# Performance work log

Measured on AMD Instinct MI355X. Metric: run time of the kernel, lower is better.

Reference implementation:

```python
import jax, jax.numpy as jnp
import numpy as np

PATCH_NUMS = (1, 2, 4, 8, 16)
BETA = 0.25
A = -0.75  # torch bicubic coefficient


def _cubic(s):
    s = abs(s)
    if s <= 1.0:
        return ((A + 2.0) * s - (A + 3.0)) * s * s + 1.0
    if s < 2.0:
        return (((s - 5.0) * s + 8.0) * s - 4.0) * A
    return 0.0


def bicubic_matrix(n_in, n_out):
    # Row-stochastic 1D resampling matrix matching torch upsample_bicubic2d
    # (align_corners=False: half-pixel centers, border index clamping).
    scale = n_in / n_out
    W = np.zeros((n_out, n_in), dtype=np.float32)
    for i in range(n_out):
        x = (i + 0.5) * scale - 0.5
        x0 = int(np.floor(x))
        t = x - x0
        for off in (-1, 0, 1, 2):
            idx = min(max(x0 + off, 0), n_in - 1)
            W[i, idx] += _cubic(t - off)
    return jnp.asarray(W)


def area_down(x, pn):
    # exact average pooling (h, w divisible by pn)
    b, c, h, w = x.shape
    kh, kw = h // pn, w // pn
    return x.reshape(b, c, pn, kh, pn, kw).mean(axis=(3, 5))


def bicubic_up(x, h_out, w_out):
    b, c, h_in, w_in = x.shape
    Wh = bicubic_matrix(h_in, h_out)  # (h_out, h_in)
    Ww = bicubic_matrix(w_in, w_out)  # (w_out, w_in)
    x = jnp.einsum('Oh,bchw->bcOw', Wh, x)
    x = jnp.einsum('Pw,bchw->bchP', Ww, x)
    return x


def vector_quantize(z, embed, beta):
    # z: (b,c,h,w); embed: (V,c)
    b, c, h, w = z.shape
    zf = z.transpose(0, 2, 3, 1).reshape(-1, c)  # (N,c)
    # squared L2 distances to codebook, (N,V)
    d = (zf * zf).sum(-1, keepdims=True) - 2.0 * zf @ embed.T + (embed * embed).sum(-1)
    idx = jnp.argmin(d, axis=1)  # (N,)
    zq = embed[idx].reshape(b, h, w, c).transpose(0, 3, 1, 2)
    sg = jax.lax.stop_gradient
    loss = beta * jnp.mean((sg(zq) - z) ** 2) + jnp.mean((zq - sg(z)) ** 2)
    zq_st = z + sg(zq - z)  # straight-through estimator
    return zq_st, idx.reshape(b, h, w), loss


def setup_inputs() -> dict:
    key = jax.random.key(0)
    k1, k2 = jax.random.split(key)
    z = jax.random.normal(k1, (256, 32, 16, 16), dtype=jnp.float32)
    embed = jax.random.normal(k2, (4096, 32), dtype=jnp.float32)
    return {"z": z, "embed": embed}


def reference(z, embed):
    b, c, h, w = z.shape
    f_rest = z
    f_hat = jnp.zeros_like(z)
    ms_idx = []
    vq_loss = jnp.float32(0.0)
    n = len(PATCH_NUMS)
    for i, pn in enumerate(PATCH_NUMS):
        z_scale = area_down(f_rest, pn) if i < n - 1 else f_rest
        z_q_scale, idx, loss_i = vector_quantize(z_scale, embed, BETA)
        z_q = bicubic_up(z_q_scale, h, w) if i < n - 1 else z_q_scale
        f_hat = f_hat + z_q
        f_rest = f_rest - z_q
        ms_idx.append(idx)
        vq_loss = vq_loss + loss_i
    vq_loss = vq_loss / n
    return (f_hat, *ms_idx, vq_loss)
```

## Files before the change

### kernel.cpp

```cpp
#include <hip/hip_runtime.h>
#include <hip/hip_bf16.h>
#include <cstdint>
#include <cstddef>


#define B_   256
#define V_   4096
#define NTOT 2097152
#define WIN  128
#define CAP  512
#define MARGIN_ 1.0f

using bf16x8 = __attribute__((ext_vector_type(8))) short;
using f32x4  = __attribute__((ext_vector_type(4))) float;

__device__ inline short f2bf(float f) {
  __hip_bfloat16 h = __float2bfloat16(f);
  return *reinterpret_cast<short*>(&h);
}
__device__ inline unsigned encf(float f) {
  unsigned u = __float_as_uint(f);
  return (u & 0x80000000u) ? ~u : (u | 0x80000000u);
}
__device__ inline float decf(unsigned u) {
  unsigned b = (u & 0x80000000u) ? (u ^ 0x80000000u) : ~u;
  return __uint_as_float(b);
}
__device__ inline int keyidx(unsigned long long k) {
  int i = (int)(unsigned)(k & 0xffffffffull);
  return min(max(i, 0), V_ - 1);
}
__device__ inline float min3f(float a, float b, float c) {
  float d;
  asm("v_min3_f32 %0, %1, %2, %3" : "=v"(d) : "v"(a), "v"(b), "v"(c));
  return d;
}

__global__ __launch_bounds__(256) void setup_kernel(
    const float* __restrict__ z, const float* __restrict__ embed,
    float* __restrict__ f_rest, float* __restrict__ zrow,
    short* __restrict__ zrowb, short* __restrict__ ebf,
    float* __restrict__ se, float* __restrict__ tables,
    float* __restrict__ loss_slots, unsigned long long* __restrict__ keys0,
    unsigned int* __restrict__ smin0)
{
  const int tid = threadIdx.x;
  const int t = blockIdx.x * 256 + tid;
  float v = z[t];
  f_rest[t] = v;

  __shared__ float sm[256];
  sm[tid] = v;
  __syncthreads();
  if (tid == 0) {
    float s = 0.f;
    for (int i = 0; i < 256; ++i) s += sm[i];
    int c = blockIdx.x & 31, b = blockIdx.x >> 5;
    float val = s * (1.0f / 256.0f);
    zrow[(size_t)b * 32 + c] = val;
    zrowb[(size_t)b * 32 + c] = f2bf(-val);
  }

  if (blockIdx.x < 16) {
    int code = blockIdx.x * 256 + tid;
    float s = 0.f;
#pragma unroll
    for (int c = 0; c < 32; ++c) {
      float e = embed[(size_t)code * 32 + c];
      ebf[(size_t)code * 32 + c] = f2bf(e);
      s += e * e;
    }
    se[code] = s;
  } else if (blockIdx.x == 16) {
    if (tid < 64) {
      int pn_i = tid >> 4;
      int o    = tid & 15;
      int pn   = 1 << pn_i;
      double scale = (double)pn / 16.0;
      double x  = (o + 0.5) * scale - 0.5;
      double x0 = floor(x);
      double tf = x - x0;
      float row[8];
#pragma unroll
      for (int h = 0; h < 8; ++h) row[h] = 0.f;
      const double A = -0.75;
#pragma unroll
      for (int off = -1; off <= 2; ++off) {
        double s = fabs(tf - (double)off);
        double cub;
        if (s <= 1.0)      cub = ((A + 2.0) * s - (A + 3.0)) * s * s + 1.0;
        else if (s < 2.0)  cub = (((s - 5.0) * s + 8.0) * s - 4.0) * A;
        else               cub = 0.0;
        int idx = (int)x0 + off;
        idx = min(max(idx, 0), pn - 1);
        row[idx] = (float)((double)row[idx] + cub);
      }
#pragma unroll
      for (int h = 0; h < 8; ++h) tables[pn_i * 128 + o * 8 + h] = row[h];
    }
  } else if (blockIdx.x == 17) {
    keys0[tid] = ~0ull;
    smin0[tid] = 0xFFFFFFFFu;
  } else if (blockIdx.x >= 20 && blockIdx.x < 60) {
    loss_slots[(blockIdx.x - 20) * 256 + tid] = 0.f;
  }
}

__global__ __launch_bounds__(256) void vq_phaseA_kernel(
    const short* __restrict__ zrowb, const short* __restrict__ ebf,
    const float* __restrict__ se, unsigned int* __restrict__ smin,
    int vchunk)
{
  __shared__ __align__(16) short elds[WIN * 40];
  __shared__ float selds[WIN];

  const int tid = threadIdx.x;
  const int lane = tid & 63, wave = tid >> 6;
  const int col = lane & 15, quad = lane >> 4;
  const int nw = blockIdx.x * 128 + wave * 32;
  const int vbase = blockIdx.y * vchunk;

  bf16x8 af[2];
#pragma unroll
  for (int f = 0; f < 2; ++f)
    af[f] = *(const bf16x8*)(zrowb + (size_t)(nw + f * 16 + col) * 32 + quad * 8);

  float mn[2][4];
#pragma unroll
  for (int f = 0; f < 2; ++f)
#pragma unroll
    for (int r = 0; r < 4; ++r) mn[f][r] = 3.4e38f;

  for (int w0 = 0; w0 < vchunk; w0 += WIN) {
    __syncthreads();
    {
      int row = tid >> 1, half = tid & 1;
      const bf16x8* src = (const bf16x8*)(ebf + (size_t)(vbase + w0 + row) * 32);
      bf16x8* dst = (bf16x8*)(elds + row * 40);
      dst[half * 2]     = src[half * 2];
      dst[half * 2 + 1] = src[half * 2 + 1];
      if (tid < WIN) selds[tid] = 0.5f * se[vbase + w0 + tid];
    }
    __syncthreads();
    for (int vv = 0; vv < WIN; vv += 16) {
      bf16x8 bf = *(const bf16x8*)(elds + (vv + col) * 40 + quad * 8);
      float sevh = selds[vv + col];
      f32x4 cin = {sevh, sevh, sevh, sevh};
#pragma unroll
      for (int f = 0; f < 2; ++f) {
        f32x4 d = __builtin_amdgcn_mfma_f32_16x16x32_bf16(af[f], bf, cin, 0, 0, 0);
#pragma unroll
        for (int r = 0; r < 4; ++r) mn[f][r] = fminf(mn[f][r], d[r]);
      }
    }
  }
#pragma unroll
  for (int f = 0; f < 2; ++f)
#pragma unroll
    for (int r = 0; r < 4; ++r) {
      float m = mn[f][r];
      m = fminf(m, __shfl_xor(m, 1, 64));
      m = fminf(m, __shfl_xor(m, 2, 64));
      m = fminf(m, __shfl_xor(m, 4, 64));
      m = fminf(m, __shfl_xor(m, 8, 64));
      mn[f][r] = m;
    }
  if (col == 0) {
#pragma unroll
    for (int f = 0; f < 2; ++f)
#pragma unroll
      for (int r = 0; r < 4; ++r)
        atomicMin(&smin[nw + f * 16 + quad * 4 + r], encf(mn[f][r]));
  }
}

__global__ __launch_bounds__(256) void vq_phaseB_kernel(
    const short* __restrict__ zrowb, const short* __restrict__ ebf,
    const float* __restrict__ se, const unsigned int* __restrict__ smin,
    const float* __restrict__ zrow, const float* __restrict__ embed,
    unsigned long long* __restrict__ keys, int vchunk, int nmax)
{
  __shared__ __align__(16) short elds[WIN * 40];
  __shared__ float selds[WIN];
  __shared__ unsigned long long clist[CAP];
  __shared__ int ccnt;

  const int tid = threadIdx.x;
  const int lane = tid & 63, wave = tid >> 6;
  const int col = lane & 15, quad = lane >> 4;
  const int nw = blockIdx.x * 128 + wave * 32;
  const int vbase = blockIdx.y * vchunk;

  if (tid == 0) ccnt = 0;
  __syncthreads();

  bf16x8 af[2];
#pragma unroll
  for (int f = 0; f < 2; ++f)
    af[f] = *(const bf16x8*)(zrowb + (size_t)(nw + f * 16 + col) * 32 + quad * 8);

  float thr[2][4];
#pragma unroll
  for (int f = 0; f < 2; ++f)
#pragma unroll
    for (int r = 0; r < 4; ++r)
      thr[f][r] = decf(smin[nw + f * 16 + quad * 4 + r]) + MARGIN_;
  float tmax = fmaxf(
      fmaxf(fmaxf(thr[0][0], thr[0][1]), fmaxf(thr[0][2], thr[0][3])),
      fmaxf(fmaxf(thr[1][0], thr[1][1]), fmaxf(thr[1][2], thr[1][3])));

  for (int w0 = 0; w0 < vchunk; w0 += WIN) {
    __syncthreads();
    {
      int row = tid >> 1, half = tid & 1;
      const bf16x8* src = (const bf16x8*)(ebf + (size_t)(vbase + w0 + row) * 32);
      bf16x8* dst = (bf16x8*)(elds + row * 40);
      dst[half * 2]     = src[half * 2];
      dst[half * 2 + 1] = src[half * 2 + 1];
      if (tid < WIN) selds[tid] = 0.5f * se[vbase + w0 + tid];
    }
    __syncthreads();
    for (int vv = 0; vv < WIN; vv += 16) {
      bf16x8 bf = *(const bf16x8*)(elds + (vv + col) * 40 + quad * 8);
      float sevh = selds[vv + col];
      f32x4 cin = {sevh, sevh, sevh, sevh};
      f32x4 dd[2];
      dd[0] = __builtin_amdgcn_mfma_f32_16x16x32_bf16(af[0], bf, cin, 0, 0, 0);
      dd[1] = __builtin_amdgcn_mfma_f32_16x16x32_bf16(af[1], bf, cin, 0, 0, 0);
      float a = min3f(dd[0][0], dd[0][1], dd[0][2]);
      float b = min3f(dd[0][3], dd[1][0], dd[1][1]);
      float c = min3f(dd[1][2], dd[1][3], a);
      if (fminf(b, c) <= tmax) {
#pragma unroll
        for (int f = 0; f < 2; ++f) {
#pragma unroll
          for (int r = 0; r < 4; ++r) {
            if (dd[f][r] <= thr[f][r]) {
              int n = nw + f * 16 + quad * 4 + r;
              int v = vbase + w0 + vv + col;
              int slot = atomicAdd(&ccnt, 1);
              if (slot < CAP) {
                clist[slot] =
                    ((unsigned long long)(unsigned)n << 32) | (unsigned)v;
              } else {
                const float* zp = zrow + (size_t)n * 32;
                const float* ep = embed + (size_t)v * 32;
                float dot = 0.f, sz = 0.f;
#pragma unroll 1
                for (int i = 0; i < 32; ++i) {
                  float zc = zp[i];
                  dot = fmaf(zc, ep[i], dot);
                  sz  = fmaf(zc, zc, sz);
                }
                float d = fmaf(-2.0f, dot, sz) + se[v];
                unsigned long long key =
                    ((unsigned long long)encf(d) << 32) | (unsigned)v;
                atomicMin(&keys[n], key);
              }
            }
          }
        }
      }
    }
  }

  __syncthreads();
  int tot = min(ccnt, CAP);
  for (int j = tid; j < tot; j += 256) {
    unsigned long long cv = clist[j];
    int n = min((int)(cv >> 32), nmax - 1);
    int v = min((int)(cv & 0xffffffffull), V_ - 1);
    const float* zp = zrow + (size_t)n * 32;
    const float* ep = embed + (size_t)v * 32;
    float dot = 0.f, sz = 0.f;
#pragma unroll
    for (int i = 0; i < 32; ++i) {
      float zc = zp[i];
      dot = fmaf(zc, ep[i], dot);
      sz  = fmaf(zc, zc, sz);
    }
    float d = fmaf(-2.0f, dot, sz) + se[v];
    unsigned long long key =
        ((unsigned long long)encf(d) << 32) | (unsigned)v;
    atomicMin(&keys[n], key);
  }
}

__global__ __launch_bounds__(256) void up_update_kernel(
    const float* __restrict__ embed, const unsigned long long* __restrict__ keys,
    const float* __restrict__ tbl, float* __restrict__ f_rest, int pn,
    float* __restrict__ zcol,
    unsigned long long* __restrict__ keys_nb, unsigned int* __restrict__ smin_nb,
    int pn_next, int n_next,
    float* __restrict__ idx_out, float* __restrict__ loss_slot)
{
  __shared__ float sm[256];
  __shared__ float sm_e[64];
  const int tid = threadIdx.x;
  const int t = blockIdx.x * 256 + tid;
  const int p = tid & 15, o = tid >> 4;
  const int c = blockIdx.x & 31, b = blockIdx.x >> 5;
  const int pn2 = pn * pn;

  float pre = f_rest[t];
  sm[tid] = pre;
  if (tid < pn2) {
    int idx = keyidx(keys[b * pn2 + tid]);
    if (c == 0) idx_out[b * pn2 + tid] = (float)idx;
    sm_e[tid] = embed[(size_t)idx * 32 + c];
  }
  __syncthreads();

  float lsum = 0.f;
  if (tid < pn2) {
    int k = 16 / pn;
    int ph = tid / pn, pw = tid - ph * pn;
    float s = 0.f;
    for (int i = 0; i < k; ++i)
      for (int j = 0; j < k; ++j)
        s += sm[(ph * k + i) * 16 + (pw * k + j)];
    float zavg = s * (1.0f / (k * k));
    float d = sm_e[tid] - zavg;
    lsum = d * d;
  }
#pragma unroll
  for (int off = 32; off > 0; off >>= 1) lsum += __shfl_down(lsum, off, 64);
  if ((tid & 63) == 0)
    atomicAdd(loss_slot + ((blockIdx.x & 127) << 4), lsum);

  const float* Wo = tbl + o * 8;
  const float* Wp = tbl + p * 8;
  float acc = 0.f;
  for (int w = 0; w < pn; ++w) {
    float inner = 0.f;
    for (int h = 0; h < pn; ++h)
      inner = fmaf(Wo[h], sm_e[h * pn + w], inner);
    acc = fmaf(Wp[w], inner, acc);
  }
  float nr = pre - acc;
  f_rest[t] = nr;

  __syncthreads();
  sm[tid] = nr;
  __syncthreads();
  const int pnn2 = pn_next * pn_next;
  if (tid < pnn2) {
    int ph = tid / pn_next, pw = tid - ph * pn_next;
    int k = 16 / pn_next;
    float s = 0.f;
    for (int i = 0; i < k; ++i)
      for (int j = 0; j < k; ++j)
        s += sm[(ph * k + i) * 16 + (pw * k + j)];
    float zavg = s * (1.0f / (k * k));
    zcol[(size_t)c * 65536 + b * pnn2 + tid] = zavg;
  }
  if (t < n_next) {
    keys_nb[t] = ~0ull;
    smin_nb[t] = 0xFFFFFFFFu;
  }
}

__global__ __launch_bounds__(256) void zpack_transpose_kernel(
    const float* __restrict__ zcol, float* __restrict__ zrow,
    short* __restrict__ zrowb)
{
  __shared__ float tile[64][33];
  const int tid = threadIdx.x;
  const int nb = blockIdx.x * 64;
  const int pt = tid & 63, cg = tid >> 6;
#pragma unroll
  for (int it = 0; it < 8; ++it) {
    int c = it * 4 + cg;
    tile[pt][c] = zcol[(size_t)c * 65536 + nb + pt];
  }
  __syncthreads();
  const int p = tid >> 2, q = tid & 3;
  float v[8];
#pragma unroll
  for (int k = 0; k < 8; ++k) v[k] = tile[p][q * 8 + k];
  float* op = zrow + (size_t)(nb + p) * 32 + q * 8;
  f32x4 lo = {v[0], v[1], v[2], v[3]};
  f32x4 hi = {v[4], v[5], v[6], v[7]};
  *(f32x4*)op = lo;
  *(f32x4*)(op + 4) = hi;
  bf16x8 bv;
#pragma unroll
  for (int k = 0; k < 8; ++k) bv[k] = f2bf(-v[k]);
  *(bf16x8*)(zrowb + (size_t)(nb + p) * 32 + q * 8) = bv;
}

__global__ __launch_bounds__(256) void final_add_kernel(
    const float* __restrict__ z, const float* __restrict__ f_rest,
    const float* __restrict__ embed, const unsigned long long* __restrict__ keys,
    float* __restrict__ f_hat, float* __restrict__ idx_out,
    float* __restrict__ loss_slot)
{
  const int tid = threadIdx.x;
  const int t = blockIdx.x * 256 + tid;
  const int c = blockIdx.x & 31, b = blockIdx.x >> 5;
  const int n = b * 256 + tid;
  int idx = keyidx(keys[n]);
  if (c == 0) idx_out[n] = (float)idx;
  float e = embed[(size_t)idx * 32 + c];
  float fr = f_rest[t];
  f_hat[t] = (z[t] - fr) + e;
  float d = e - fr;
  float lsum = d * d;
#pragma unroll
  for (int off = 32; off > 0; off >>= 1) lsum += __shfl_down(lsum, off, 64);
  if ((tid & 63) == 0)
    atomicAdd(loss_slot + ((blockIdx.x & 127) << 4), lsum);
}

__global__ __launch_bounds__(128) void loss_final_kernel(
    const float* __restrict__ loss_slots, float* __restrict__ out_loss)
{
  __shared__ float lred[2];
  const int tid = threadIdx.x;
  const float numel[5] = {8192.f, 32768.f, 131072.f, 524288.f, 2097152.f};
  float tot = 0.f;
  for (int s = 0; s < 5; ++s) {
    float x = loss_slots[s * 2048 + tid * 16];
#pragma unroll
    for (int off = 32; off > 0; off >>= 1) x += __shfl_down(x, off, 64);
    if ((tid & 63) == 0) lred[tid >> 6] = x;
    __syncthreads();
    if (tid == 0) {
      float m = (lred[0] + lred[1]) / numel[s];
      tot += 0.25f * m + m;
    }
    __syncthreads();
  }
  if (tid == 0) out_loss[0] = tot / 5.f;
}

extern "C" void kernel_launch(void* const* d_in, const int* in_sizes, int n_in,
                              void* d_out, int out_size, void* d_ws, size_t ws_size,
                              hipStream_t stream)
{
  const float* z     = (const float*)d_in[0];
  const float* embed = (const float*)d_in[1];
  float* out = (float*)d_out;
  float* ws  = (float*)d_ws;

  float* f_rest  = ws;
  float* zrow    = ws + 2097152;
  short* zrowb   = (short*)(ws + 4194304);
  short* ebf     = (short*)(ws + 5242880);
  float* se      = ws + 5308416;
  unsigned int* smin0 = (unsigned int*)(ws + 5312512);
  unsigned int* smin1 = (unsigned int*)(ws + 5378048);
  unsigned long long* keys0 = (unsigned long long*)(ws + 5394432);
  unsigned long long* keys1 = (unsigned long long*)(ws + 5525504);
  float* loss_slots = ws + 5558272;
  float* tables     = ws + 5568512;

  float* zcol = out;

  unsigned long long* keysb[2] = {keys0, keys1};
  unsigned int*       sminb[2] = {smin0, smin1};

  setup_kernel<<<NTOT / 256, 256, 0, stream>>>(z, embed, f_rest, zrow, zrowb,
                                               ebf, se, tables, loss_slots,
                                               keys0, smin0);

  const int PN[5]  = {1, 2, 4, 8, 16};
  const int NVC[5] = {32, 32, 32, 16, 16};
  int idx_off = NTOT;
  for (int i = 0; i < 5; ++i) {
    int pn = PN[i];
    int N  = B_ * pn * pn;
    int vchunk = V_ / NVC[i];
    unsigned long long* kb = keysb[i & 1];
    unsigned int*       sb = sminb[i & 1];
    dim3 g(N / 128, NVC[i]);
    vq_phaseA_kernel<<<g, 256, 0, stream>>>(zrowb, ebf, se, sb, vchunk);
    vq_phaseB_kernel<<<g, 256, 0, stream>>>(zrowb, ebf, se, sb, zrow, embed,
                                            kb, vchunk, N);
    if (i < 4) {
      int pnn = PN[i + 1];
      int n_next = B_ * pnn * pnn;
      up_update_kernel<<<NTOT / 256, 256, 0, stream>>>(
          embed, kb, tables + i * 128, f_rest, pn,
          zcol, keysb[(i + 1) & 1], sminb[(i + 1) & 1],
          pnn, n_next, out + idx_off, loss_slots + i * 2048);
      zpack_transpose_kernel<<<n_next / 64, 256, 0, stream>>>(zcol, zrow,
                                                              zrowb);
    } else {
      final_add_kernel<<<NTOT / 256, 256, 0, stream>>>(
          z, f_rest, embed, kb, out, out + idx_off, loss_slots + 4 * 2048);
    }
    idx_off += N;
  }
  loss_final_kernel<<<1, 128, 0, stream>>>(loss_slots, out + 2184448);
}
```

Before: 385.9 us.

## Compact candidate rows per vocab chunk before phase B on large scales

Phase A now also records each row's per-chunk minimum distance for the two largest scales. A new compaction kernel builds, per vocabulary chunk, a worklist of rows whose chunk minimum lies within the margin of the global minimum. A worklist-driven phase B then recomputes the MFMA distances only for those (row, chunk) pairs. This is meant to avoid redundant phase-B work on chunks that cannot hold the argmin, at the cost of an extra kernel launch, extra global writes, and atomics.

```diff
diff --git a/kernel.cpp b/kernel.cpp
--- a/kernel.cpp
+++ b/kernel.cpp
@@ -9,6 +9,7 @@
 #define NTOT 2097152
 #define WIN  128
 #define CAP  512
+#define CAPW 1024
 #define MARGIN_ 1.0f
 
 using bf16x8 = __attribute__((ext_vector_type(8))) short;
@@ -42,7 +43,7 @@
     short* __restrict__ zrowb, short* __restrict__ ebf,
     float* __restrict__ se, float* __restrict__ tables,
     float* __restrict__ loss_slots, unsigned long long* __restrict__ keys0,
-    unsigned int* __restrict__ smin0)
+    unsigned int* __restrict__ smin0, int* __restrict__ cnt0)
 {
   const int tid = threadIdx.x;
   const int t = blockIdx.x * 256 + tid;
@@ -101,6 +102,8 @@
   } else if (blockIdx.x == 17) {
     keys0[tid] = ~0ull;
     smin0[tid] = 0xFFFFFFFFu;
+  } else if (blockIdx.x == 18) {
+    if (tid < 32) cnt0[tid] = 0;
   } else if (blockIdx.x >= 20 && blockIdx.x < 60) {
     loss_slots[(blockIdx.x - 20) * 256 + tid] = 0.f;
   }
@@ -109,7 +112,7 @@
 __global__ __launch_bounds__(256) void vq_phaseA_kernel(
     const short* __restrict__ zrowb, const short* __restrict__ ebf,
     const float* __restrict__ se, unsigned int* __restrict__ smin,
-    int vchunk)
+    int vchunk, unsigned int* __restrict__ chunkmin, int N)
 {
   __shared__ __align__(16) short elds[WIN * 40];
   __shared__ float selds[WIN];
@@ -169,8 +172,12 @@
 #pragma unroll
     for (int f = 0; f < 2; ++f)
 #pragma unroll
-      for (int r = 0; r < 4; ++r)
-        atomicMin(&smin[nw + f * 16 + quad * 4 + r], encf(mn[f][r]));
+      for (int r = 0; r < 4; ++r) {
+        unsigned e = encf(mn[f][r]);
+        int n = nw + f * 16 + quad * 4 + r;
+        atomicMin(&smin[n], e);
+        if (chunkmin) chunkmin[(size_t)blockIdx.y * N + n] = e;
+      }
   }
 }
 
@@ -286,6 +293,147 @@
   }
 }
 
+__global__ __launch_bounds__(256) void compact_kernel(
+    const unsigned int* __restrict__ smin,
+    const unsigned int* __restrict__ chunkmin, int N, int nvc,
+    int* __restrict__ cnt, int* __restrict__ list)
+{
+  const int n = blockIdx.x * 256 + threadIdx.x;
+  const int lane = threadIdx.x & 63;
+  const float thr = decf(smin[n]) + MARGIN_;
+  for (int y = 0; y < nvc; ++y) {
+    bool q = decf(chunkmin[(size_t)y * N + n]) <= thr;
+    unsigned long long m = __ballot(q);
+    int base = 0;
+    if (lane == 0 && m) base = atomicAdd(&cnt[y], (int)__popcll(m));
+    base = __shfl(base, 0, 64);
+    if (q) {
+      int pos = base + (int)__popcll(m & ((1ull << lane) - 1ull));
+      list[(size_t)y * N + pos] = n;
+    }
+  }
+}
+
+__global__ __launch_bounds__(256) void vq_phaseB_wl_kernel(
+    const short* __restrict__ zrowb, const short* __restrict__ ebf,
+    const float* __restrict__ se, const unsigned int* __restrict__ smin,
+    const float* __restrict__ zrow, const float* __restrict__ embed,
+    unsigned long long* __restrict__ keys, int vchunk, int N,
+    const int* __restrict__ cnt, const int* __restrict__ list)
+{
+  __shared__ __align__(16) short elds[WIN * 40];
+  __shared__ float selds[WIN];
+  __shared__ unsigned long long clist[CAPW];
+  __shared__ int ptls[128];
+  __shared__ int ccnt;
+
+  const int tid = threadIdx.x;
+  const int lane = tid & 63, wave = tid >> 6;
+  const int col = lane & 15, quad = lane >> 4;
+  const int y = blockIdx.y;
+  const int vbase = y * vchunk;
+  const int total = cnt[y];
+
+  if (tid == 0) ccnt = 0;
+
+  for (int base = blockIdx.x * 128; base < total; base += gridDim.x * 128) {
+    __syncthreads();
+    if (tid < 128)
+      ptls[tid] = list[(size_t)y * N + min(base + tid, total - 1)];
+    __syncthreads();
+
+    bf16x8 af[2];
+    float thr[2][4];
+#pragma unroll
+    for (int f = 0; f < 2; ++f) {
+      int pm = ptls[wave * 32 + f * 16 + col];
+      af[f] = *(const bf16x8*)(zrowb + (size_t)pm * 32 + quad * 8);
+#pragma unroll
+      for (int r = 0; r < 4; ++r)
+        thr[f][r] = decf(smin[ptls[wave * 32 + f * 16 + quad * 4 + r]]) + MARGIN_;
+    }
+    float tmax = fmaxf(
+        fmaxf(fmaxf(thr[0][0], thr[0][1]), fmaxf(thr[0][2], thr[0][3])),
+        fmaxf(fmaxf(thr[1][0], thr[1][1]), fmaxf(thr[1][2], thr[1][3])));
+
+    for (int w0 = 0; w0 < vchunk; w0 += WIN) {
+      __syncthreads();
+      {
+        int row = tid >> 1, half = tid & 1;
+        const bf16x8* src = (const bf16x8*)(ebf + (size_t)(vbase + w0 + row) * 32);
+        bf16x8* dst = (bf16x8*)(elds + row * 40);
+        dst[half * 2]     = src[half * 2];
+        dst[half * 2 + 1] = src[half * 2 + 1];
+        if (tid < WIN) selds[tid] = 0.5f * se[vbase + w0 + tid];
+      }
+      __syncthreads();
+      for (int vv = 0; vv < WIN; vv += 16) {
+        bf16x8 bf = *(const bf16x8*)(elds + (vv + col) * 40 + quad * 8);
+        float sevh = selds[vv + col];
+        f32x4 cin = {sevh, sevh, sevh, sevh};
+        f32x4 dd[2];
+        dd[0] = __builtin_amdgcn_mfma_f32_16x16x32_bf16(af[0], bf, cin, 0, 0, 0);
+        dd[1] = __builtin_amdgcn_mfma_f32_16x16x32_bf16(af[1], bf, cin, 0, 0, 0);
+        float a = min3f(dd[0][0], dd[0][1], dd[0][2]);
+        float b = min3f(dd[0][3], dd[1][0], dd[1][1]);
+        float c = min3f(dd[1][2], dd[1][3], a);
+        if (fminf(b, c) <= tmax) {
+#pragma unroll
+          for (int f = 0; f < 2; ++f) {
+#pragma unroll
+            for (int r = 0; r < 4; ++r) {
+              if (dd[f][r] <= thr[f][r]) {
+                int n = ptls[wave * 32 + f * 16 + quad * 4 + r];
+                int v = vbase + w0 + vv + col;
+                int slot = atomicAdd(&ccnt, 1);
+                if (slot < CAPW) {
+                  clist[slot] =
+                      ((unsigned long long)(unsigned)n << 32) | (unsigned)v;
+                } else {
+                  const float* zp = zrow + (size_t)n * 32;
+                  const float* ep = embed + (size_t)v * 32;
+                  float dot = 0.f, sz = 0.f;
+#pragma unroll 1
+                  for (int i = 0; i < 32; ++i) {
+                    float zc = zp[i];
+                    dot = fmaf(zc, ep[i], dot);
+                    sz  = fmaf(zc, zc, sz);
+                  }
+                  float d = fmaf(-2.0f, dot, sz) + se[v];
+                  unsigned long long key =
+                      ((unsigned long long)encf(d) << 32) | (unsigned)v;
+                  atomicMin(&keys[n], key);
+                }
+              }
+            }
+          }
+        }
+      }
+    }
+  }
+
+  __syncthreads();
+  int tot = min(ccnt, CAPW);
+  for (int j = tid; j < tot; j += 256) {
+    unsigned long long cv = clist[j];
+    int n = min((int)(cv >> 32), N - 1);
+    int v = min((int)(cv & 0xffffffffull), V_ - 1);
+    const float* zp = zrow + (size_t)n * 32;
+    const float* ep = embed + (size_t)v * 32;
+    float dot = 0.f, sz = 0.f;
+#pragma unroll
+    for (int i = 0; i < 32; ++i) {
+      float zc = zp[i];
+      dot = fmaf(zc, ep[i], dot);
+      sz  = fmaf(zc, zc, sz);
+    }
+    float d = fmaf(-2.0f, dot, sz) + se[v];
+    unsigned long long key =
+        ((unsigned long long)encf(d) << 32) | (unsigned)v;
+    atomicMin(&keys[n], key);
+  }
+}
+
 __global__ __launch_bounds__(256) void up_update_kernel(
     const float* __restrict__ embed, const unsigned long long* __restrict__ keys,
     const float* __restrict__ tbl, float* __restrict__ f_rest, int pn,
@@ -454,6 +602,9 @@
   unsigned long long* keys1 = (unsigned long long*)(ws + 5525504);
   float* loss_slots = ws + 5558272;
   float* tables     = ws + 5568512;
+  int*   cnt0       = (int*)(ws + 5569024);
+  unsigned int* chunkmin = (unsigned int*)(ws + 5569056);
+  int*   list       = (int*)(ws + 6617632);
 
   float* zcol = out;
 
@@ -462,7 +613,7 @@
 
   setup_kernel<<<NTOT / 256, 256, 0, stream>>>(z, embed, f_rest, zrow, zrowb,
                                                ebf, se, tables, loss_slots,
-                                               keys0, smin0);
+                                               keys0, smin0, cnt0);
 
   const int PN[5]  = {1, 2, 4, 8, 16};
   const int NVC[5] = {32, 32, 32, 16, 16};
@@ -474,9 +625,20 @@
     unsigned long long* kb = keysb[i & 1];
     unsigned int*       sb = sminb[i & 1];
     dim3 g(N / 128, NVC[i]);
-    vq_phaseA_kernel<<<g, 256, 0, stream>>>(zrowb, ebf, se, sb, vchunk);
-    vq_phaseB_kernel<<<g, 256, 0, stream>>>(zrowb, ebf, se, sb, zrow, embed,
-                                            kb, vchunk, N);
+    vq_phaseA_kernel<<<g, 256, 0, stream>>>(zrowb, ebf, se, sb, vchunk,
+                                            (i >= 3) ? chunkmin : nullptr, N);
+    if (i < 3) {
+      vq_phaseB_kernel<<<g, 256, 0, stream>>>(zrowb, ebf, se, sb, zrow, embed,
+                                              kb, vchunk, N);
+    } else {
+      int* cnt = cnt0 + (i - 3) * 16;
+      compact_kernel<<<N / 256, 256, 0, stream>>>(sb, chunkmin, N, NVC[i],
+                                                  cnt, list);
+      dim3 gw(32, NVC[i]);
+      vq_phaseB_wl_kernel<<<gw, 256, 0, stream>>>(zrowb, ebf, se, sb, zrow,
+                                                  embed, kb, vchunk, N,
+                                                  cnt, list);
+    }
     if (i < 4) {
       int pnn = PN[i + 1];
       int n_next = B_ * pnn * pnn;
```

Result: slower. 612.5 us (+58.7%).
